# Kernel tuning notes

Hardware: AMD Instinct MI355X
Metric: run time of the kernel (lower is better)

The kernel has to match this reference:

```python
import jax, jax.numpy as jnp
import numpy as np


def setup_inputs() -> dict:
    key = jax.random.key(0)
    k1, k2, k3 = jax.random.split(key, 3)
    B, H, S, D = 4, 16, 1024, 64
    return {
        "query": jax.random.normal(k1, (B, H, S, D), dtype=jnp.float32),
        "key": jax.random.normal(k2, (B, H, D, S), dtype=jnp.float32),  # pre-transposed K
        "scale_factor": 8,  # sqrt(head_dim)
        "attention_mask": jnp.zeros((S, S), dtype=jnp.float32),
        "value": jax.random.normal(k3, (B, H, S, D), dtype=jnp.float32),
    }


def reference(query, key, scale_factor, attention_mask, value):
    # Batched equivalent of the per-(b,h) Python loop:
    # scores = Q @ K^T / scale + mask; probs = softmax(scores); out = probs @ V
    scores = jnp.matmul(query, key) / scale_factor  # [B,H,S,S]
    if attention_mask is not None:
        scores = scores + attention_mask  # broadcast [S,S] over [B,H,S,S]
    probs = jax.nn.softmax(scores, axis=-1)
    return jnp.matmul(probs, value)  # [B,H,S,D]
```

## Files before the change

kernel.cpp:

```cpp
#include <hip/hip_runtime.h>

#define BH  64
#define SEQ 1024
#define DIM 64
#define KT  64

typedef __attribute__((ext_vector_type(8))) short  short8;
typedef __attribute__((ext_vector_type(4))) float  floatx4;

__device__ __forceinline__ ushort f2bf(float x) {
    union { float f; uint u; } v; v.f = x;
    uint r = v.u + 0x7FFFu + ((v.u >> 16) & 1u);
    return (ushort)(r >> 16);
}
__device__ __forceinline__ uint pack2(float lo, float hi) {
    return (uint)f2bf(lo) | ((uint)f2bf(hi) << 16);
}
__device__ __forceinline__ void gld_lds16(const void* g, void* l) {
    __builtin_amdgcn_global_load_lds(
        (const __attribute__((address_space(1))) unsigned int*)g,
        (__attribute__((address_space(3))) unsigned int*)l, 16, 0, 0);
}


__global__ __launch_bounds__(256) void prep_kv_kernel(
    const float* __restrict__ Kin,
    const float* __restrict__ Vin,
    ushort* __restrict__ Kbf, ushort* __restrict__ Vbf)
{
    __shared__ float tile[64][65];
    const int t    = threadIdx.x;
    const int head = blockIdx.y;
    const int s0   = blockIdx.x * 64;
    const int p    = t & 7;

    if (blockIdx.z == 0) {
        const float* ip = Kin + (size_t)head * DIM * SEQ;
#pragma unroll
        for (int i = 0; i < 4; ++i) {
            const int d = (t >> 4) + i * 16;
            const int c = (t & 15) * 4;
            float4 v = *(const float4*)(ip + (size_t)d * SEQ + s0 + c);
            tile[d][c]     = v.x; tile[d][c + 1] = v.y;
            tile[d][c + 2] = v.z; tile[d][c + 3] = v.w;
        }
        __syncthreads();
        char* op = (char*)(Kbf + (size_t)head * SEQ * DIM);
#pragma unroll
        for (int i = 0; i < 2; ++i) {
            const int s  = (t >> 3) + i * 32;
            const int dg = (p ^ (s & 7)) * 8;
            uint4 wv;
            wv.x = pack2(tile[dg + 0][s], tile[dg + 1][s]);
            wv.y = pack2(tile[dg + 2][s], tile[dg + 3][s]);
            wv.z = pack2(tile[dg + 4][s], tile[dg + 5][s]);
            wv.w = pack2(tile[dg + 6][s], tile[dg + 7][s]);
            *(uint4*)(op + (size_t)(s0 + s) * 128 + p * 16) = wv;
        }
    } else {
        const float* ip = Vin + (size_t)head * SEQ * DIM;
#pragma unroll
        for (int i = 0; i < 4; ++i) {
            const int ss = (t >> 4) + i * 16;
            const int c  = (t & 15) * 4;
            float4 v = *(const float4*)(ip + (size_t)(s0 + ss) * DIM + c);
            tile[ss][c]     = v.x; tile[ss][c + 1] = v.y;
            tile[ss][c + 2] = v.z; tile[ss][c + 3] = v.w;
        }
        __syncthreads();
        char* op = (char*)(Vbf + (size_t)head * SEQ * DIM) + (size_t)(s0 >> 6) * 8192;
#pragma unroll
        for (int i = 0; i < 2; ++i) {
            const int d  = (t >> 3) + i * 32;
            const int sg = (p ^ (d & 7)) * 8;
            uint4 wv;
            wv.x = pack2(tile[sg + 0][d], tile[sg + 1][d]);
            wv.y = pack2(tile[sg + 2][d], tile[sg + 3][d]);
            wv.z = pack2(tile[sg + 4][d], tile[sg + 5][d]);
            wv.w = pack2(tile[sg + 6][d], tile[sg + 7][d]);
            *(uint4*)(op + (size_t)d * 128 + p * 16) = wv;
        }
    }
}

__global__ __launch_bounds__(256, 5) void mha_mfma2_kernel(
    const float*  __restrict__ Q,
    const ushort* __restrict__ Kbf,
    const int*    __restrict__ scale_p,
    const float*  __restrict__ mask,
    const ushort* __restrict__ Vbf,
    float*        __restrict__ O)
{
    __shared__ __align__(16) ushort Ks[KT * 64];
    __shared__ __align__(16) ushort Vt[DIM * 64];
    __shared__ __align__(16) ushort Ps[4 * 16 * 64];

    const int t    = threadIdx.x;
    const int lane = t & 63, w = t >> 6;
    const int li   = lane & 15, quad = lane >> 4;
    const int lx   = li & 7;
    const int bh   = blockIdx.x >> 4;
    const int q0   = (blockIdx.x & 15) * 64;

    const float inv_scale = 1.0f / (float)scale_p[0];

    {
        const float* Qg = Q + ((size_t)bh * SEQ + q0) * DIM;
        const int rr = t >> 4, cc = (t & 15) * 4;
#pragma unroll
        for (int i = 0; i < 4; ++i) {
            const int row = rr + 16 * i;
            float4 v = *(const float4*)(Qg + (size_t)row * DIM + cc);
            uint2 pw; pw.x = pack2(v.x, v.y); pw.y = pack2(v.z, v.w);
            *(uint2*)((char*)Ks + row * 128 + (((cc >> 3) ^ (row & 7)) * 16)
                      + (cc & 7) * 2) = pw;
        }
    }
    __syncthreads();
    const char* qrow = (const char*)Ks + (w * 16 + li) * 128;
    const short8 qa0 = *(const short8*)(qrow + ((quad ^ lx) * 16));
    const short8 qa1 = *(const short8*)(qrow + (((4 + quad) ^ lx) * 16));

    floatx4 o[4] = {floatx4{0,0,0,0}, floatx4{0,0,0,0},
                    floatx4{0,0,0,0}, floatx4{0,0,0,0}};
    float l_r[4] = {0.f, 0.f, 0.f, 0.f};

    const char* KgH = (const char*)(Kbf + (size_t)bh * SEQ * DIM);
    const char* VgH = (const char*)(Vbf + (size_t)bh * SEQ * DIM);
    const int so = w * 2048 + lane * 16;
    char* ksd = (char*)Ks + w * 2048;
    char* vtd = (char*)Vt + w * 2048;
    char* psw = (char*)Ps + w * 2048;

    const float* mrow = mask + (size_t)(q0 + w * 16 + quad * 4) * SEQ + li;

    for (int kt = 0; kt < SEQ / KT; ++kt) {
        const int key0 = kt * KT;
        __syncthreads();
        const char* kg = KgH + kt * 8192 + so;
        const char* vg = VgH + kt * 8192 + so;
        gld_lds16(kg,        ksd);
        gld_lds16(kg + 1024, ksd + 1024);
        gld_lds16(vg,        vtd);
        gld_lds16(vg + 1024, vtd + 1024);
        __syncthreads();

        float mv[16];
#pragma unroll
        for (int n = 0; n < 4; ++n)
#pragma unroll
            for (int r = 0; r < 4; ++r)
                mv[n * 4 + r] = mrow[(size_t)r * SEQ + key0 + n * 16];

        floatx4 c[4] = {floatx4{0,0,0,0}, floatx4{0,0,0,0},
                        floatx4{0,0,0,0}, floatx4{0,0,0,0}};
#pragma unroll
        for (int n = 0; n < 4; ++n) {
            const char* krow = (const char*)Ks + (n * 16 + li) * 128;
            short8 b0 = *(const short8*)(krow + ((quad ^ lx) * 16));
            short8 b1 = *(const short8*)(krow + (((4 + quad) ^ lx) * 16));
            c[n] = __builtin_amdgcn_mfma_f32_16x16x32_bf16(qa0, b0, c[n], 0, 0, 0);
            c[n] = __builtin_amdgcn_mfma_f32_16x16x32_bf16(qa1, b1, c[n], 0, 0, 0);
        }

#pragma unroll
        for (int n = 0; n < 4; ++n)
#pragma unroll
            for (int r = 0; r < 4; ++r) {
                float s = fminf(fmaf(c[n][r], inv_scale, mv[n * 4 + r]), 80.f);
                float p = __expf(s);
                l_r[r] += p;
                const int row = quad * 4 + r, col = n * 16 + li;
                *(ushort*)(psw + row * 128 + (((col >> 3) ^ (row & 7)) * 16)
                           + (col & 7) * 2) = f2bf(p);
            }

#pragma unroll
        for (int kk = 0; kk < 2; ++kk) {
            short8 a = *(const short8*)(psw + li * 128 + (((kk * 4 + quad) ^ lx) * 16));
#pragma unroll
            for (int n = 0; n < 4; ++n) {
                const char* vrow = (const char*)Vt + (n * 16 + li) * 128;
                short8 b = *(const short8*)(vrow + (((kk * 4 + quad) ^ lx) * 16));
                o[n] = __builtin_amdgcn_mfma_f32_16x16x32_bf16(a, b, o[n], 0, 0, 0);
            }
        }
    }

#pragma unroll
    for (int off = 1; off < 16; off <<= 1)
#pragma unroll
        for (int r = 0; r < 4; ++r)
            l_r[r] += __shfl_xor(l_r[r], off);

    float* Og = O + ((size_t)bh * SEQ + q0) * DIM;
#pragma unroll
    for (int r = 0; r < 4; ++r) {
        const float inv_l = 1.0f / l_r[r];
#pragma unroll
        for (int n = 0; n < 4; ++n)
            Og[(size_t)(w * 16 + quad * 4 + r) * DIM + n * 16 + li] = o[n][r] * inv_l;
    }
}

extern "C" void kernel_launch(void* const* d_in, const int* in_sizes, int n_in,
                              void* d_out, int out_size, void* d_ws, size_t ws_size,
                              hipStream_t stream) {
    const float* Q     = (const float*)d_in[0];
    const float* K     = (const float*)d_in[1];
    const int*   scale = (const int*)d_in[2];
    const float* mask  = (const float*)d_in[3];
    const float* V     = (const float*)d_in[4];
    float*       Out   = (float*)d_out;

    ushort* Kbf = (ushort*)d_ws;
    ushort* Vbf = Kbf + (size_t)BH * SEQ * DIM;

    prep_kv_kernel<<<dim3(SEQ / 64, BH, 2), 256, 0, stream>>>(K, V, Kbf, Vbf);
    mha_mfma2_kernel<<<dim3(BH * (SEQ / KT)), 256, 0, stream>>>(Q, Kbf, scale, mask, Vbf, Out);
}
```

Baseline: 138.3 us.

## Double-buffer K/V LDS tiles and prefetch the next tile and mask during compute

Splits the K and V shared-memory tiles into two buffers. The next tile's global-to-LDS loads and mask values are issued before computing on the current tile, with a manual vmcnt wait and raw barriers replacing the two syncthreads per iteration. It also raises wave priority around the MFMA sections and lowers the occupancy hint from 5 to 4. The aim is to hide global load latency behind matrix work, at the cost of doubled LDS for K/V, more registers and fragile hand-tuned waitcnt values. On the last iteration the prefetch wraps around to tile 0, which adds redundant loads.

```diff
diff --git a/kernel.cpp b/kernel.cpp
--- a/kernel.cpp
+++ b/kernel.cpp
@@ -4,6 +4,7 @@
 #define SEQ 1024
 #define DIM 64
 #define KT  64
+#define NT  (SEQ / KT)
 
 typedef __attribute__((ext_vector_type(8))) short  short8;
 typedef __attribute__((ext_vector_type(4))) float  floatx4;
@@ -83,7 +84,7 @@
     }
 }
 
-__global__ __launch_bounds__(256, 5) void mha_mfma2_kernel(
+__global__ __launch_bounds__(256, 4) void mha_mfma2_kernel(
     const float*  __restrict__ Q,
     const ushort* __restrict__ Kbf,
     const int*    __restrict__ scale_p,
@@ -91,8 +92,8 @@
     const ushort* __restrict__ Vbf,
     float*        __restrict__ O)
 {
-    __shared__ __align__(16) ushort Ks[KT * 64];
-    __shared__ __align__(16) ushort Vt[DIM * 64];
+    __shared__ __align__(16) ushort Ks0[KT * 64], Ks1[KT * 64];
+    __shared__ __align__(16) ushort Vt0[DIM * 64], Vt1[DIM * 64];
     __shared__ __align__(16) ushort Ps[4 * 16 * 64];
 
     const int t    = threadIdx.x;
@@ -112,14 +113,15 @@
             const int row = rr + 16 * i;
             float4 v = *(const float4*)(Qg + (size_t)row * DIM + cc);
             uint2 pw; pw.x = pack2(v.x, v.y); pw.y = pack2(v.z, v.w);
-            *(uint2*)((char*)Ks + row * 128 + (((cc >> 3) ^ (row & 7)) * 16)
+            *(uint2*)((char*)Ks0 + row * 128 + (((cc >> 3) ^ (row & 7)) * 16)
                       + (cc & 7) * 2) = pw;
         }
     }
     __syncthreads();
-    const char* qrow = (const char*)Ks + (w * 16 + li) * 128;
+    const char* qrow = (const char*)Ks0 + (w * 16 + li) * 128;
     const short8 qa0 = *(const short8*)(qrow + ((quad ^ lx) * 16));
     const short8 qa1 = *(const short8*)(qrow + (((4 + quad) ^ lx) * 16));
+    __syncthreads();
 
     floatx4 o[4] = {floatx4{0,0,0,0}, floatx4{0,0,0,0},
                     floatx4{0,0,0,0}, floatx4{0,0,0,0}};
@@ -128,46 +130,73 @@
     const char* KgH = (const char*)(Kbf + (size_t)bh * SEQ * DIM);
     const char* VgH = (const char*)(Vbf + (size_t)bh * SEQ * DIM);
     const int so = w * 2048 + lane * 16;
-    char* ksd = (char*)Ks + w * 2048;
-    char* vtd = (char*)Vt + w * 2048;
-    char* psw = (char*)Ps + w * 2048;
+    char* ksd0 = (char*)Ks0 + w * 2048;
+    char* ksd1 = (char*)Ks1 + w * 2048;
+    char* vtd0 = (char*)Vt0 + w * 2048;
+    char* vtd1 = (char*)Vt1 + w * 2048;
+    char* psw  = (char*)Ps  + w * 2048;
 
     const float* mrow = mask + (size_t)(q0 + w * 16 + quad * 4) * SEQ + li;
 
-    for (int kt = 0; kt < SEQ / KT; ++kt) {
-        const int key0 = kt * KT;
-        __syncthreads();
-        const char* kg = KgH + kt * 8192 + so;
-        const char* vg = VgH + kt * 8192 + so;
-        gld_lds16(kg,        ksd);
-        gld_lds16(kg + 1024, ksd + 1024);
-        gld_lds16(vg,        vtd);
-        gld_lds16(vg + 1024, vtd + 1024);
-        __syncthreads();
-
-        float mv[16];
+    float mvc[16], mvn[16];
+#pragma unroll
+    for (int n = 0; n < 4; ++n)
+#pragma unroll
+        for (int r = 0; r < 4; ++r)
+            mvc[n * 4 + r] = mrow[(size_t)r * SEQ + n * 16];
+    gld_lds16(KgH + so,        ksd0);
+    gld_lds16(KgH + so + 1024, ksd0 + 1024);
+    gld_lds16(VgH + so,        vtd0);
+    gld_lds16(VgH + so + 1024, vtd0 + 1024);
+    __builtin_amdgcn_sched_barrier(0);
+
+#pragma unroll 2
+    for (int kt = 0; kt < NT; ++kt) {
+        const int c = kt & 1;
+        const char* ksb = c ? (const char*)Ks1 : (const char*)Ks0;
+        const char* vtb = c ? (const char*)Vt1 : (const char*)Vt0;
+        char* ksdN = c ? ksd0 : ksd1;
+        char* vtdN = c ? vtd0 : vtd1;
+
+        __builtin_amdgcn_s_barrier();
+
+        const int kn = (kt + 1) & (NT - 1);
 #pragma unroll
         for (int n = 0; n < 4; ++n)
 #pragma unroll
             for (int r = 0; r < 4; ++r)
-                mv[n * 4 + r] = mrow[(size_t)r * SEQ + key0 + n * 16];
-
-        floatx4 c[4] = {floatx4{0,0,0,0}, floatx4{0,0,0,0},
-                        floatx4{0,0,0,0}, floatx4{0,0,0,0}};
+                mvn[n * 4 + r] = mrow[(size_t)r * SEQ + kn * KT + n * 16];
+        {
+            const char* kg = KgH + kn * 8192 + so;
+            const char* vg = VgH + kn * 8192 + so;
+            gld_lds16(kg,        ksdN);
+            gld_lds16(kg + 1024, ksdN + 1024);
+            gld_lds16(vg,        vtdN);
+            gld_lds16(vg + 1024, vtdN + 1024);
+        }
+        __builtin_amdgcn_sched_barrier(0);
+        asm volatile("s_waitcnt vmcnt(20)" ::: "memory");
+        __builtin_amdgcn_sched_barrier(0);
+        __builtin_amdgcn_s_barrier();
+
+        floatx4 cfr[4] = {floatx4{0,0,0,0}, floatx4{0,0,0,0},
+                          floatx4{0,0,0,0}, floatx4{0,0,0,0}};
+        __builtin_amdgcn_s_setprio(1);
 #pragma unroll
         for (int n = 0; n < 4; ++n) {
-            const char* krow = (const char*)Ks + (n * 16 + li) * 128;
+            const char* krow = ksb + (n * 16 + li) * 128;
             short8 b0 = *(const short8*)(krow + ((quad ^ lx) * 16));
             short8 b1 = *(const short8*)(krow + (((4 + quad) ^ lx) * 16));
-            c[n] = __builtin_amdgcn_mfma_f32_16x16x32_bf16(qa0, b0, c[n], 0, 0, 0);
-            c[n] = __builtin_amdgcn_mfma_f32_16x16x32_bf16(qa1, b1, c[n], 0, 0, 0);
-        }
+            cfr[n] = __builtin_amdgcn_mfma_f32_16x16x32_bf16(qa0, b0, cfr[n], 0, 0, 0);
+            cfr[n] = __builtin_amdgcn_mfma_f32_16x16x32_bf16(qa1, b1, cfr[n], 0, 0, 0);
+        }
+        __builtin_amdgcn_s_setprio(0);
 
 #pragma unroll
         for (int n = 0; n < 4; ++n)
 #pragma unroll
             for (int r = 0; r < 4; ++r) {
-                float s = fminf(fmaf(c[n][r], inv_scale, mv[n * 4 + r]), 80.f);
+                float s = fminf(fmaf(cfr[n][r], inv_scale, mvc[n * 4 + r]), 80.f);
                 float p = __expf(s);
                 l_r[r] += p;
                 const int row = quad * 4 + r, col = n * 16 + li;
@@ -175,16 +204,21 @@
                            + (col & 7) * 2) = f2bf(p);
             }
 
+        __builtin_amdgcn_s_setprio(1);
 #pragma unroll
         for (int kk = 0; kk < 2; ++kk) {
             short8 a = *(const short8*)(psw + li * 128 + (((kk * 4 + quad) ^ lx) * 16));
 #pragma unroll
             for (int n = 0; n < 4; ++n) {
-                const char* vrow = (const char*)Vt + (n * 16 + li) * 128;
+                const char* vrow = vtb + (n * 16 + li) * 128;
                 short8 b = *(const short8*)(vrow + (((kk * 4 + quad) ^ lx) * 16));
                 o[n] = __builtin_amdgcn_mfma_f32_16x16x32_bf16(a, b, o[n], 0, 0, 0);
             }
         }
+        __builtin_amdgcn_s_setprio(0);
+
+#pragma unroll
+        for (int j = 0; j < 16; ++j) mvc[j] = mvn[j];
     }
 
 #pragma unroll
```

Result: no change. 136.3 us (-1.5%).
